# Optimization experiments

Hardware: AMD Instinct MI355X
Metric: run time of the kernel (lower is better)

The kernel has to match this reference:

```python
import jax, jax.numpy as jnp
import numpy as np

# Dims: N tokens, top_k K, E experts, d_model D, expert hidden H
N, K, E, D, H = 4096, 2, 8, 1024, 1024


def setup_inputs() -> dict:
    key = jax.random.key(0)
    k1, k2, k3, k4, k5, k6 = jax.random.split(key, 6)
    x = jax.random.normal(k1, (N, D), dtype=jnp.float32)
    expert_indices = jax.random.randint(k2, (N, K), 0, E, dtype=jnp.int32)
    ew = jax.random.uniform(k3, (N, K), dtype=jnp.float32)
    expert_weights = ew / ew.sum(-1, keepdims=True)  # router probs over top-k
    # histogram consistent with expert_indices (computed by the router in the real model)
    batch_size_per_expert = jnp.bincount(expert_indices.reshape(-1), length=E).astype(jnp.int32)
    w1 = jax.random.normal(k4, (E, D, H), dtype=jnp.float32) * (D ** -0.5)
    w3 = jax.random.normal(k5, (E, D, H), dtype=jnp.float32) * (D ** -0.5)
    w2 = jax.random.normal(k6, (E, H, D), dtype=jnp.float32) * (H ** -0.5)
    return {
        "x": x,
        "expert_weights": expert_weights,
        "expert_indices": expert_indices,
        "batch_size_per_expert": batch_size_per_expert,
        "w1": w1,
        "w2": w2,
        "w3": w3,
    }


def reference(x, expert_weights, expert_indices, batch_size_per_expert, w1, w2, w3):
    """Dropless MoE: sort token-copies by expert, grouped-GEMM SwiGLU, unpermute+combine."""
    nk = N * K
    flat_idx = expert_indices.reshape(nk)               # (N*K,)
    order = jnp.argsort(flat_idx)                        # stable sort -> permutation into expert order
    x_perm = x[order // K]                               # (N*K, D) gather source token per copy
    gs = batch_size_per_expert.astype(jnp.int32)         # grouped-GEMM group sizes, sums to N*K
    # per-expert SwiGLU MLP via grouped GEMM (rows of x_perm are contiguous per expert)
    h = jax.nn.silu(jax.lax.ragged_dot(x_perm, w1, gs)) * jax.lax.ragged_dot(x_perm, w3, gs)  # (N*K, H)
    out_perm = jax.lax.ragged_dot(h, w2, gs)             # (N*K, D)
    # unpermute: scatter rows back to original (token, k) order
    out_flat = jnp.zeros_like(x_perm).at[order].set(out_perm)  # (N*K, D)
    # weighted combine over top-k copies
    out = jnp.einsum("nk,nkd->nd", expert_weights, out_flat.reshape(N, K, D))
    return out
```

## Files before the change

kernel.cpp:

```cpp
#include <hip/hip_runtime.h>
#include <hip/hip_bf16.h>
#include <stdint.h>

#define N_TOK   4096
#define TOPK    2
#define N_EXP   8
#define D_MODEL 1024
#define H_DIM   1024
#define NK      (N_TOK * TOPK)
#define MAX_TILES 72

typedef __attribute__((ext_vector_type(8))) short bf16x8;
typedef __attribute__((ext_vector_type(4))) float f32x4;
typedef __attribute__((ext_vector_type(4))) unsigned int uint32x4;
typedef unsigned short bfbits;

__device__ inline bfbits f2bf_bits(float f) {
  union { float f; unsigned int u; } v; v.f = f;
  unsigned int r = v.u + 0x7FFFu + ((v.u >> 16) & 1u);
  return (bfbits)(r >> 16);
}
__device__ inline float bf2f(unsigned short u) {
  union { unsigned int u; float f; } v; v.u = ((unsigned int)u) << 16;
  return v.f;
}

__device__ inline void glds16(const bfbits* g, bfbits* l) {
  __builtin_amdgcn_global_load_lds(
      (const __attribute__((address_space(1))) void*)g,
      (__attribute__((address_space(3))) void*)l, 16, 0, 0);
}

__global__ __launch_bounds__(256, 2) void prepass_kernel(
    const float* __restrict__ x, const int* __restrict__ eidx,
    const int* __restrict__ bspe,
    const float* __restrict__ w1, const float* __restrict__ w2,
    const float* __restrict__ w3,
    bfbits* __restrict__ w1t, bfbits* __restrict__ w2t,
    bfbits* __restrict__ w3t, bfbits* __restrict__ xb,
    int* __restrict__ meta, int* __restrict__ row_src,
    int* __restrict__ pos_of) {
  int z = blockIdx.z;
  int tid = threadIdx.x;

  if (z >= 1 && z <= 6) {
    int flat = (z - 1) * 128 + blockIdx.y * 16 + blockIdx.x;
    int mat = flat >> 5;
    int tile = flat & 31;
    int r0 = (tile >> 3) * 256;
    int c0 = (tile & 7) * 128;
    const size_t MAT = (size_t)1024 * 1024;
    const float* src; bfbits* dst;
    if (mat < 8)       { src = w1 + (size_t)mat * MAT;        dst = w1t + (size_t)mat * MAT; }
    else if (mat < 16) { src = w3 + (size_t)(mat - 8) * MAT;  dst = w3t + (size_t)(mat - 8) * MAT; }
    else               { src = w2 + (size_t)(mat - 16) * MAT; dst = w2t + (size_t)(mat - 16) * MAT; }

    __shared__ __align__(16) bfbits Ts[128 * 256];
    char* tsb = (char*)Ts;

    int q = tid & 31;
    int p = tid >> 5;
    int xo = (q & 31) << 4;

#pragma unroll
    for (int it = 0; it < 4; it++) {
      int o8 = it * 8 + p;
      float4 v[8];
#pragma unroll
      for (int k = 0; k < 8; k++)
        v[k] = *(const float4*)&src[(size_t)(r0 + o8 * 8 + k) * 1024 + c0 + q * 4];
      const float* vf = (const float*)v;
#pragma unroll
      for (int j = 0; j < 4; j++) {
        uint32x4 pk;
        pk.x = (unsigned int)f2bf_bits(vf[0 * 4 + j]) | ((unsigned int)f2bf_bits(vf[1 * 4 + j]) << 16);
        pk.y = (unsigned int)f2bf_bits(vf[2 * 4 + j]) | ((unsigned int)f2bf_bits(vf[3 * 4 + j]) << 16);
        pk.z = (unsigned int)f2bf_bits(vf[4 * 4 + j]) | ((unsigned int)f2bf_bits(vf[5 * 4 + j]) << 16);
        pk.w = (unsigned int)f2bf_bits(vf[6 * 4 + j]) | ((unsigned int)f2bf_bits(vf[7 * 4 + j]) << 16);
        *(uint32x4*)(tsb + (q * 4 + j) * 512 + ((o8 * 16) ^ xo)) = pk;
      }
    }
    __syncthreads();
    int m = tid & 31;
    int g = tid >> 5;
#pragma unroll
    for (int it = 0; it < 16; it++) {
      int a = it * 8 + g;
      int xr = ((a >> 2) & 31) << 4;
      uint32x4 d = *(const uint32x4*)(tsb + a * 512 + ((m * 16) ^ xr));
      *(uint32x4*)&dst[(size_t)(c0 + a) * 1024 + r0 + m * 8] = d;
    }
  } else if (z >= 7) {
    int idx = (z - 7) * 128 + blockIdx.y * 16 + blockIdx.x;
    const float4* xv = (const float4*)x;
    ushort4* xo = (ushort4*)xb;
#pragma unroll
    for (int qq = 0; qq < 4; qq++) {
      int fi = idx * 1024 + qq * 256 + tid;
      float4 v = xv[fi];
      ushort4 o;
      o.x = f2bf_bits(v.x); o.y = f2bf_bits(v.y);
      o.z = f2bf_bits(v.z); o.w = f2bf_bits(v.w);
      xo[fi] = o;
    }
  } else {
    if (blockIdx.x != 0 || blockIdx.y != 0) return;
    __shared__ int sm[162];
    __shared__ int scnt[N_EXP];
    if (tid == 0) {
      int acc = 0, nt = 0;
      for (int e = 0; e < N_EXP; e++) {
        sm[e] = acc;
        int g = bspe[e];
        for (int tt = 0; tt * 128 < g; tt++) {
          sm[18 + nt] = e;
          sm[90 + nt] = acc + tt * 128;
          nt++;
        }
        acc += g;
      }
      sm[8] = acc;
      sm[17] = nt;
      for (int i = nt; i < MAX_TILES; i++) { sm[18 + i] = 0; sm[90 + i] = 0; }
    }
    if (tid < N_EXP) scnt[tid] = 0;
    __syncthreads();
    int4 eb[8];
#pragma unroll
    for (int q = 0; q < 8; q++) eb[q] = ((const int4*)eidx)[q * 256 + tid];
#pragma unroll
    for (int q = 0; q < 8; q++) {
      int ii = (q * 256 + tid) * 4;
      const int* ev = (const int*)&eb[q];
#pragma unroll
      for (int j = 0; j < 4; j++) {
        int e = ev[j];
        int p = sm[e] + atomicAdd(&scnt[e], 1);
        row_src[p] = ii + j;
        pos_of[ii + j] = p;
      }
    }
    if (tid < 162) meta[tid] = sm[tid];
  }
}

__global__ __launch_bounds__(256, 4) void gemm_swiglu_kernel(
    const bfbits* __restrict__ xb, const bfbits* __restrict__ w1t,
    const bfbits* __restrict__ w3t, const int* __restrict__ row_src,
    const int* __restrict__ meta, bfbits* __restrict__ hb) {
  int nt = meta[17];
  int bt = blockIdx.y;
  if (bt >= nt) return;
  int e = meta[18 + bt];
  int row0 = meta[90 + bt];
  int rows_end = meta[e + 1];
  int n0 = blockIdx.x * 64;

  __shared__ __align__(16) bfbits As[128 * 64];
  __shared__ __align__(16) bfbits B1s[64 * 64];
  __shared__ __align__(16) bfbits B3s[64 * 64];

  int tid = threadIdx.x, lane = tid & 63, wv = tid >> 6;
  int r8 = lane >> 3, jl = lane & 7;
  int jg = jl ^ r8;

  const bfbits* gp[8]; bfbits* lp[8];
  for (int j = 0; j < 8; j++) {
    int s = wv * 8 + j;
    if (s < 16) {
      int tok = row_src[row0 + s * 8 + r8] >> 1;
      gp[j] = xb + (size_t)tok * D_MODEL + jg * 8;
      lp[j] = As + s * 512;
    } else if (s < 24) {
      int b = s - 16;
      gp[j] = w1t + ((size_t)e * H_DIM + n0 + b * 8 + r8) * D_MODEL + jg * 8;
      lp[j] = B1s + b * 512;
    } else {
      int b = s - 24;
      gp[j] = w3t + ((size_t)e * H_DIM + n0 + b * 8 + r8) * D_MODEL + jg * 8;
      lp[j] = B3s + b * 512;
    }
  }

  const f32x4 fzero = {0.f, 0.f, 0.f, 0.f};
  f32x4 accg[4][2], accu[4][2];
  for (int i = 0; i < 4; i++)
    for (int j = 0; j < 2; j++) { accg[i][j] = fzero; accu[i][j] = fzero; }

  int mw = (wv & 1) * 64, nwv = (wv >> 1) * 32;
  int qd = lane >> 4, lr = lane & 15, lr7 = lr & 7;

  for (int kk = 0; kk < D_MODEL / 64; kk++) {
    int ko = kk * 64;
    for (int j = 0; j < 8; j++) glds16(gp[j] + ko, lp[j]);
    __syncthreads();
    for (int ks = 0; ks < 2; ks++) {
      int sb = ((ks * 4 + qd) ^ lr7) << 3;
      bf16x8 af[4], b1f[2], b3f[2];
      for (int mi = 0; mi < 4; mi++)
        af[mi] = *(const bf16x8*)&As[(mw + mi * 16 + lr) * 64 + sb];
      for (int ni = 0; ni < 2; ni++) {
        b1f[ni] = *(const bf16x8*)&B1s[(nwv + ni * 16 + lr) * 64 + sb];
        b3f[ni] = *(const bf16x8*)&B3s[(nwv + ni * 16 + lr) * 64 + sb];
      }
      for (int mi = 0; mi < 4; mi++)
        for (int ni = 0; ni < 2; ni++) {
          accg[mi][ni] = __builtin_amdgcn_mfma_f32_16x16x32_bf16(af[mi], b1f[ni], accg[mi][ni], 0, 0, 0);
          accu[mi][ni] = __builtin_amdgcn_mfma_f32_16x16x32_bf16(af[mi], b3f[ni], accu[mi][ni], 0, 0, 0);
        }
    }
    __syncthreads();
  }

  for (int mi = 0; mi < 4; mi++) {
    int rbase = row0 + mw + mi * 16 + qd * 4;
    for (int r = 0; r < 4; r++) {
      int grow = rbase + r;
      if (grow < rows_end) {
        for (int ni = 0; ni < 2; ni++) {
          float gg = accg[mi][ni][r], u = accu[mi][ni][r];
          float h = gg / (1.f + __expf(-gg)) * u;
          hb[(size_t)grow * H_DIM + n0 + nwv + ni * 16 + lr] = f2bf_bits(h);
        }
      }
    }
  }
}

__global__ __launch_bounds__(256, 3) void gemm_out_kernel(
    const bfbits* __restrict__ hb, const bfbits* __restrict__ w2t,
    const int* __restrict__ meta, bfbits* __restrict__ out_perm) {
  int nt = meta[17];
  int bt = blockIdx.y;
  if (bt >= nt) return;
  int e = meta[18 + bt];
  int row0 = meta[90 + bt];
  int rows_end = meta[e + 1];
  int n0 = blockIdx.x * 128;

  __shared__ __align__(16) bfbits As[128 * 64];
  __shared__ __align__(16) bfbits Bs[128 * 64];

  int tid = threadIdx.x, lane = tid & 63, wv = tid >> 6;
  int r8 = lane >> 3, jl = lane & 7;
  int jg = jl ^ r8;

  const bfbits* gp[8]; bfbits* lp[8];
  for (int j = 0; j < 8; j++) {
    int s = wv * 8 + j;
    if (s < 16) {
      gp[j] = hb + (size_t)(row0 + s * 8 + r8) * H_DIM + jg * 8;
      lp[j] = As + s * 512;
    } else {
      int b = s - 16;
      gp[j] = w2t + ((size_t)e * D_MODEL + n0 + b * 8 + r8) * H_DIM + jg * 8;
      lp[j] = Bs + b * 512;
    }
  }

  const f32x4 fzero = {0.f, 0.f, 0.f, 0.f};
  f32x4 acc[4][4];
  for (int i = 0; i < 4; i++)
    for (int j = 0; j < 4; j++) acc[i][j] = fzero;

  int mw = (wv & 1) * 64, nw = (wv >> 1) * 64;
  int qd = lane >> 4, lr = lane & 15, lr7 = lr & 7;

  for (int kk = 0; kk < H_DIM / 64; kk++) {
    int ko = kk * 64;
    for (int j = 0; j < 8; j++) glds16(gp[j] + ko, lp[j]);
    __syncthreads();
    for (int ks = 0; ks < 2; ks++) {
      int sb = ((ks * 4 + qd) ^ lr7) << 3;
      bf16x8 af[4], bfr[4];
      for (int mi = 0; mi < 4; mi++)
        af[mi] = *(const bf16x8*)&As[(mw + mi * 16 + lr) * 64 + sb];
      for (int ni = 0; ni < 4; ni++)
        bfr[ni] = *(const bf16x8*)&Bs[(nw + ni * 16 + lr) * 64 + sb];
      for (int mi = 0; mi < 4; mi++)
        for (int ni = 0; ni < 4; ni++)
          acc[mi][ni] = __builtin_amdgcn_mfma_f32_16x16x32_bf16(af[mi], bfr[ni], acc[mi][ni], 0, 0, 0);
    }
    __syncthreads();
  }

  for (int mi = 0; mi < 4; mi++) {
    int rbase = row0 + mw + mi * 16 + qd * 4;
    for (int r = 0; r < 4; r++) {
      int grow = rbase + r;
      if (grow < rows_end) {
        for (int ni = 0; ni < 4; ni++)
          out_perm[(size_t)grow * D_MODEL + n0 + nw + ni * 16 + lr] = f2bf_bits(acc[mi][ni][r]);
      }
    }
  }
}

__global__ __launch_bounds__(256) void combine_kernel(
    const ushort4* __restrict__ out_perm, const int* __restrict__ pos_of,
    const float* __restrict__ ew, float4* __restrict__ out) {
  int tid = threadIdx.x;
#pragma unroll
  for (int q = 0; q < 4; q++) {
    int i = blockIdx.x * 1024 + q * 256 + tid;
    int tok = i >> 8;
    int col = i & 255;
    int p0 = pos_of[2 * tok], p1 = pos_of[2 * tok + 1];
    float w0 = ew[2 * tok], w1 = ew[2 * tok + 1];
    ushort4 a = out_perm[(size_t)p0 * 256 + col];
    ushort4 b = out_perm[(size_t)p1 * 256 + col];
    float4 o;
    o.x = w0 * bf2f(a.x) + w1 * bf2f(b.x);
    o.y = w0 * bf2f(a.y) + w1 * bf2f(b.y);
    o.z = w0 * bf2f(a.z) + w1 * bf2f(b.z);
    o.w = w0 * bf2f(a.w) + w1 * bf2f(b.w);
    out[i] = o;
  }
}

extern "C" void kernel_launch(void* const* d_in, const int* in_sizes, int n_in,
                              void* d_out, int out_size, void* d_ws, size_t ws_size,
                              hipStream_t stream) {
  const float* x  = (const float*)d_in[0];
  const float* ew = (const float*)d_in[1];
  const int* eidx = (const int*)d_in[2];
  const int* bspe = (const int*)d_in[3];
  const float* w1 = (const float*)d_in[4];
  const float* w2 = (const float*)d_in[5];
  const float* w3 = (const float*)d_in[6];
  float* out = (float*)d_out;

  char* ws = (char*)d_ws;
  const size_t MB = 1024 * 1024;
  bfbits* w1t   = (bfbits*)(ws);
  bfbits* w3t   = (bfbits*)(ws + 16 * MB);
  bfbits* w2t   = (bfbits*)(ws + 32 * MB);
  bfbits* xb    = (bfbits*)(ws + 48 * MB);
  bfbits* hb    = (bfbits*)(ws + 56 * MB);
  bfbits* out_perm = (bfbits*)(ws);
  int* row_src  = (int*)(ws + 72 * MB);
  int* pos_of   = (int*)(ws + 72 * MB + 32 * 1024);
  int* meta     = (int*)(ws + 72 * MB + 64 * 1024);

  prepass_kernel<<<dim3(16, 8, 15), 256, 0, stream>>>(
      x, eidx, bspe, w1, w2, w3, w1t, w2t, w3t, xb, meta, row_src, pos_of);
  gemm_swiglu_kernel<<<dim3(H_DIM / 64, MAX_TILES), 256, 0, stream>>>(
      xb, w1t, w3t, row_src, meta, hb);
  gemm_out_kernel<<<dim3(D_MODEL / 128, MAX_TILES), 256, 0, stream>>>(
      hb, w2t, meta, out_perm);
  combine_kernel<<<(N_TOK * D_MODEL / 4) / 1024, 256, 0, stream>>>(
      (const ushort4*)out_perm, pos_of, ew, (float4*)out);
}
```

Before: 242.2 us.

## Move w2 bf16 transpose-convert from prepass into the SwiGLU GEMM launch

The fp32-to-bf16 transposed conversion of the w2 weights moves out of the prepass kernel and into extra blocks of the first grouped-GEMM launch, using smaller 128x128 tiles. The goal is to overlap the memory-bound w2 conversion with the compute-bound SwiGLU GEMM and to shorten the serial prepass. Shared memory is merged into one buffer reused by both paths. The risk is that the conversion blocks compete with the GEMM blocks for bandwidth and CU slots, and that block scheduling order may place them late.

```diff
diff --git a/kernel.cpp b/kernel.cpp
--- a/kernel.cpp
+++ b/kernel.cpp
@@ -34,16 +34,14 @@
 __global__ __launch_bounds__(256, 2) void prepass_kernel(
     const float* __restrict__ x, const int* __restrict__ eidx,
     const int* __restrict__ bspe,
-    const float* __restrict__ w1, const float* __restrict__ w2,
-    const float* __restrict__ w3,
-    bfbits* __restrict__ w1t, bfbits* __restrict__ w2t,
-    bfbits* __restrict__ w3t, bfbits* __restrict__ xb,
+    const float* __restrict__ w1, const float* __restrict__ w3,
+    bfbits* __restrict__ w1t, bfbits* __restrict__ w3t, bfbits* __restrict__ xb,
     int* __restrict__ meta, int* __restrict__ row_src,
     int* __restrict__ pos_of) {
   int z = blockIdx.z;
   int tid = threadIdx.x;
 
-  if (z >= 1 && z <= 6) {
+  if (z >= 1 && z <= 4) {
     int flat = (z - 1) * 128 + blockIdx.y * 16 + blockIdx.x;
     int mat = flat >> 5;
     int tile = flat & 31;
@@ -51,9 +49,8 @@
     int c0 = (tile & 7) * 128;
     const size_t MAT = (size_t)1024 * 1024;
     const float* src; bfbits* dst;
-    if (mat < 8)       { src = w1 + (size_t)mat * MAT;        dst = w1t + (size_t)mat * MAT; }
-    else if (mat < 16) { src = w3 + (size_t)(mat - 8) * MAT;  dst = w3t + (size_t)(mat - 8) * MAT; }
-    else               { src = w2 + (size_t)(mat - 16) * MAT; dst = w2t + (size_t)(mat - 16) * MAT; }
+    if (mat < 8) { src = w1 + (size_t)mat * MAT;       dst = w1t + (size_t)mat * MAT; }
+    else         { src = w3 + (size_t)(mat - 8) * MAT; dst = w3t + (size_t)(mat - 8) * MAT; }
 
     __shared__ __align__(16) bfbits Ts[128 * 256];
     char* tsb = (char*)Ts;
@@ -90,8 +87,8 @@
       uint32x4 d = *(const uint32x4*)(tsb + a * 512 + ((m * 16) ^ xr));
       *(uint32x4*)&dst[(size_t)(c0 + a) * 1024 + r0 + m * 8] = d;
     }
-  } else if (z >= 7) {
-    int idx = (z - 7) * 128 + blockIdx.y * 16 + blockIdx.x;
+  } else if (z >= 5) {
+    int idx = (z - 5) * 128 + blockIdx.y * 16 + blockIdx.x;
     const float4* xv = (const float4*)x;
     ushort4* xo = (ushort4*)xb;
 #pragma unroll
@@ -147,20 +144,68 @@
 __global__ __launch_bounds__(256, 4) void gemm_swiglu_kernel(
     const bfbits* __restrict__ xb, const bfbits* __restrict__ w1t,
     const bfbits* __restrict__ w3t, const int* __restrict__ row_src,
-    const int* __restrict__ meta, bfbits* __restrict__ hb) {
+    const int* __restrict__ meta, bfbits* __restrict__ hb,
+    const float* __restrict__ w2, bfbits* __restrict__ w2t) {
+  __shared__ __align__(16) bfbits SMEM[16384];
+  int tid = threadIdx.x;
+  int by = blockIdx.y;
+
+  if (by >= MAX_TILES) {
+    int flat = (by - MAX_TILES) * 16 + blockIdx.x;
+    int mat = flat >> 6;
+    int tile = flat & 63;
+    int r0 = (tile >> 3) * 128;
+    int c0 = (tile & 7) * 128;
+    const size_t MAT = (size_t)1024 * 1024;
+    const float* src = w2 + (size_t)mat * MAT;
+    bfbits* dst = w2t + (size_t)mat * MAT;
+    char* tsb = (char*)SMEM;
+
+    int q = tid & 31, p = tid >> 5;
+    int xo = (q & 15) << 4;
+#pragma unroll
+    for (int it = 0; it < 2; it++) {
+      int o8 = it * 8 + p;
+      float4 v[8];
+#pragma unroll
+      for (int k = 0; k < 8; k++)
+        v[k] = *(const float4*)&src[(size_t)(r0 + o8 * 8 + k) * 1024 + c0 + q * 4];
+      const float* vf = (const float*)v;
+#pragma unroll
+      for (int j = 0; j < 4; j++) {
+        uint32x4 pk;
+        pk.x = (unsigned int)f2bf_bits(vf[0 * 4 + j]) | ((unsigned int)f2bf_bits(vf[1 * 4 + j]) << 16);
+        pk.y = (unsigned int)f2bf_bits(vf[2 * 4 + j]) | ((unsigned int)f2bf_bits(vf[3 * 4 + j]) << 16);
+        pk.z = (unsigned int)f2bf_bits(vf[4 * 4 + j]) | ((unsigned int)f2bf_bits(vf[5 * 4 + j]) << 16);
+        pk.w = (unsigned int)f2bf_bits(vf[6 * 4 + j]) | ((unsigned int)f2bf_bits(vf[7 * 4 + j]) << 16);
+        *(uint32x4*)(tsb + (q * 4 + j) * 256 + ((o8 * 16) ^ xo)) = pk;
+      }
+    }
+    __syncthreads();
+    int m = tid & 15, g = tid >> 4;
+#pragma unroll
+    for (int it = 0; it < 8; it++) {
+      int a = it * 16 + g;
+      int xr = ((a >> 2) & 15) << 4;
+      uint32x4 d = *(const uint32x4*)(tsb + a * 256 + ((m * 16) ^ xr));
+      *(uint32x4*)&dst[(size_t)(c0 + a) * 1024 + r0 + m * 8] = d;
+    }
+    return;
+  }
+
   int nt = meta[17];
-  int bt = blockIdx.y;
+  int bt = by;
   if (bt >= nt) return;
   int e = meta[18 + bt];
   int row0 = meta[90 + bt];
   int rows_end = meta[e + 1];
   int n0 = blockIdx.x * 64;
 
-  __shared__ __align__(16) bfbits As[128 * 64];
-  __shared__ __align__(16) bfbits B1s[64 * 64];
-  __shared__ __align__(16) bfbits B3s[64 * 64];
-
-  int tid = threadIdx.x, lane = tid & 63, wv = tid >> 6;
+  bfbits* As  = SMEM;
+  bfbits* B1s = SMEM + 8192;
+  bfbits* B3s = SMEM + 12288;
+
+  int lane = tid & 63, wv = tid >> 6;
   int r8 = lane >> 3, jl = lane & 7;
   int jg = jl ^ r8;
 
@@ -342,10 +387,10 @@
   int* pos_of   = (int*)(ws + 72 * MB + 32 * 1024);
   int* meta     = (int*)(ws + 72 * MB + 64 * 1024);
 
-  prepass_kernel<<<dim3(16, 8, 15), 256, 0, stream>>>(
-      x, eidx, bspe, w1, w2, w3, w1t, w2t, w3t, xb, meta, row_src, pos_of);
-  gemm_swiglu_kernel<<<dim3(H_DIM / 64, MAX_TILES), 256, 0, stream>>>(
-      xb, w1t, w3t, row_src, meta, hb);
+  prepass_kernel<<<dim3(16, 8, 13), 256, 0, stream>>>(
+      x, eidx, bspe, w1, w3, w1t, w3t, xb, meta, row_src, pos_of);
+  gemm_swiglu_kernel<<<dim3(H_DIM / 64, MAX_TILES + 32), 256, 0, stream>>>(
+      xb, w1t, w3t, row_src, meta, hb, w2, w2t);
   gemm_out_kernel<<<dim3(D_MODEL / 128, MAX_TILES), 256, 0, stream>>>(
       hb, w2t, meta, out_perm);
   combine_kernel<<<(N_TOK * D_MODEL / 4) / 1024, 256, 0, stream>>>(
```

Result: no change. 239.3 us (-1.2%).
